# Optimization experiments

Measured on AMD Instinct MI355X. Metric: run time of the kernel, lower is better.

Reference implementation:

```python
import jax, jax.numpy as jnp
import numpy as np

B, H, W, DIM = 16, 64, 64, 512
GH, GW = 8, 8
NH = 16
HD = DIM // NH
POS = DIM // 16  # DynamicPosBias pos_dim = (dim//4)//4 = 32
EPS = 1e-5


def setup_inputs() -> dict:
    key = jax.random.key(0)
    ks = jax.random.split(key, 12)
    w = lambda k, s: jax.random.normal(k, s, jnp.float32) * 0.02
    f32 = jnp.float32
    return {
        "x": jax.random.normal(ks[0], (B, H * W, DIM), f32),
        "norm1_g": jnp.ones((DIM,), f32), "norm1_b": jnp.zeros((DIM,), f32),
        "qkv_w": w(ks[1], (3 * DIM, DIM)), "qkv_b": jnp.zeros((3 * DIM,), f32),
        "proj_w": w(ks[2], (DIM, DIM)), "proj_b": jnp.zeros((DIM,), f32),
        "pos_w0": w(ks[3], (POS, 2)), "pos_b0": jnp.zeros((POS,), f32),
        "pos_ln0_g": jnp.ones((POS,), f32), "pos_ln0_b": jnp.zeros((POS,), f32),
        "pos_w1": w(ks[4], (POS, POS)), "pos_b1": jnp.zeros((POS,), f32),
        "pos_ln1_g": jnp.ones((POS,), f32), "pos_ln1_b": jnp.zeros((POS,), f32),
        "pos_w2": w(ks[5], (POS, POS)), "pos_b2": jnp.zeros((POS,), f32),
        "pos_ln2_g": jnp.ones((POS,), f32), "pos_ln2_b": jnp.zeros((POS,), f32),
        "pos_w3": w(ks[6], (NH, POS)), "pos_b3": jnp.zeros((NH,), f32),
        "norm2_g": jnp.ones((DIM,), f32), "norm2_b": jnp.zeros((DIM,), f32),
        "mlp_w1": w(ks[7], (4 * DIM, DIM)), "mlp_b1": jnp.zeros((4 * DIM,), f32),
        "mlp_w2": w(ks[8], (DIM, 4 * DIM)), "mlp_b2": jnp.zeros((DIM,), f32),
    }


def _ln(x, g, b):
    m = jnp.mean(x, -1, keepdims=True)
    v = jnp.mean(jnp.square(x - m), -1, keepdims=True)
    return (x - m) * jax.lax.rsqrt(v + EPS) * g + b


def _rel_bias_tables():
    # relative coordinate table [(2GH-1)*(2GW-1), 2]
    ph = jnp.arange(1 - GH, GH)
    pw = jnp.arange(1 - GW, GW)
    biases = jnp.stack(jnp.meshgrid(ph, pw, indexing="ij")).reshape(2, -1).T.astype(jnp.float32)
    # relative position index [GH*GW, GH*GW]
    coords = jnp.stack(jnp.meshgrid(jnp.arange(GH), jnp.arange(GW), indexing="ij")).reshape(2, -1)
    rel = (coords[:, :, None] - coords[:, None, :]).transpose(1, 2, 0)  # [N,N,2]
    idx = (rel[..., 0] + GH - 1) * (2 * GW - 1) + (rel[..., 1] + GW - 1)
    return biases, idx


def reference(x, norm1_g, norm1_b, qkv_w, qkv_b, proj_w, proj_b,
              pos_w0, pos_b0, pos_ln0_g, pos_ln0_b,
              pos_w1, pos_b1, pos_ln1_g, pos_ln1_b,
              pos_w2, pos_b2, pos_ln2_g, pos_ln2_b,
              pos_w3, pos_b3, norm2_g, norm2_b,
              mlp_w1, mlp_b1, mlp_w2, mlp_b2):
    biases, rel_idx = _rel_bias_tables()
    Ng = GH * GW
    scale = HD ** -0.5

    shortcut = x
    h = _ln(x, norm1_g, norm1_b).reshape(B, H, W, DIM)
    # use_lda=True: long-distance (strided) grouping
    h = h.reshape(B, GH, H // GH, GW, W // GW, DIM).transpose(0, 2, 4, 1, 3, 5)
    h = h.reshape(B * (H * W) // Ng, Ng, DIM)  # [G, Ng, C]

    # attention
    qkv = h @ qkv_w.T + qkv_b
    qkv = qkv.reshape(-1, Ng, 3, NH, HD).transpose(2, 0, 3, 1, 4)  # [3,G,NH,Ng,HD]
    q, k, v = qkv[0], qkv[1], qkv[2]
    attn = jnp.einsum("ghnd,ghmd->ghnm", q * scale, k)

    # dynamic position bias MLP on the coordinate table
    p = jax.nn.relu(_ln(biases @ pos_w0.T + pos_b0, pos_ln0_g, pos_ln0_b))
    p = jax.nn.relu(_ln(p @ pos_w1.T + pos_b1, pos_ln1_g, pos_ln1_b))
    p = jax.nn.relu(_ln(p @ pos_w2.T + pos_b2, pos_ln2_g, pos_ln2_b))
    p = p @ pos_w3.T + pos_b3  # [(2GH-1)(2GW-1), NH]
    rel_bias = p[rel_idx].transpose(2, 0, 1)  # [NH, Ng, Ng]

    attn = jax.nn.softmax(attn + rel_bias[None], axis=-1)
    o = jnp.einsum("ghnm,ghmd->ghnd", attn, v)
    o = o.transpose(0, 2, 1, 3).reshape(-1, Ng, DIM)
    o = o @ proj_w.T + proj_b

    # ungroup (inverse of lda grouping)
    o = o.reshape(B, H // GH, W // GW, GH, GW, DIM)
    o = o.transpose(0, 3, 1, 4, 2, 5).reshape(B, H * W, DIM)

    x = shortcut + o
    m = _ln(x, norm2_g, norm2_b)
    m = jax.nn.gelu(m @ mlp_w1.T + mlp_b1, approximate=False)
    m = m @ mlp_w2.T + mlp_b2
    return x + m
```

## Files before the change

### kernel.cpp

```cpp
#include <hip/hip_runtime.h>
#include <hip/hip_bf16.h>

typedef __bf16 bf16;
typedef __bf16 bf16x8 __attribute__((ext_vector_type(8)));
typedef __bf16 bf16x4 __attribute__((ext_vector_type(4)));
typedef float f32x4_t __attribute__((ext_vector_type(4)));

static constexpr int kDIM = 512;

static constexpr size_t OFF_QKVW = 0;
static constexpr size_t OFF_PROJW = 1572864;
static constexpr size_t OFF_W1   = 2097152;
static constexpr size_t OFF_W2   = 4194304;
static constexpr size_t OFF_PTAB = 6291456;
static constexpr size_t OFF_A    = 8388608;
static constexpr size_t OFF_B    = 276824064;

typedef __attribute__((address_space(3))) uint32_t lds_u32_t;
typedef __attribute__((address_space(1))) const uint32_t glb_u32_t;
#define ASYNC_COPY16(gp, lp) __builtin_amdgcn_global_load_lds((glb_u32_t*)(gp), (lds_u32_t*)(lp), 16, 0, 0)
#define WAITV0() asm volatile("s_waitcnt vmcnt(0)" ::: "memory")

__global__ void cast_fp8_k(const float* __restrict__ in, unsigned char* __restrict__ out, int n4)
{
    int i = blockIdx.x * blockDim.x + threadIdx.x;
    if (i < n4) {
        float4 v = ((const float4*)in)[i];
        int p = __builtin_amdgcn_cvt_pk_fp8_f32(v.x * 64.0f, v.y * 64.0f, 0, false);
        p = __builtin_amdgcn_cvt_pk_fp8_f32(v.z * 64.0f, v.w * 64.0f, p, true);
        ((unsigned int*)out)[i] = (unsigned int)p;
    }
}

template<int GROUP>
__global__ __launch_bounds__(256)
void ln_k(const float* __restrict__ x, const float* __restrict__ gw,
          const float* __restrict__ bw, unsigned char* __restrict__ out)
{
    const int t = blockIdx.x * 4 + (threadIdx.x >> 6);
    const int lane = threadIdx.x & 63;
    const float* xp = x + (size_t)t * kDIM + lane * 8;
    float4 p0 = *(const float4*)xp;
    float4 p1 = *(const float4*)(xp + 4);
    float v[8] = {p0.x, p0.y, p0.z, p0.w, p1.x, p1.y, p1.z, p1.w};
    float s = 0.f;
#pragma unroll
    for (int i = 0; i < 8; ++i) s += v[i];
#pragma unroll
    for (int off = 32; off > 0; off >>= 1) s += __shfl_xor(s, off);
    const float mean = s * (1.0f / 512.0f);
    float q = 0.f;
#pragma unroll
    for (int i = 0; i < 8; ++i) { float d = v[i] - mean; q += d * d; }
#pragma unroll
    for (int off = 32; off > 0; off >>= 1) q += __shfl_xor(q, off);
    const float rstd = rsqrtf(q * (1.0f / 512.0f) + 1e-5f);
    size_t orow;
    if (GROUP) {
        int b = t >> 12, r = (t >> 6) & 63, c = t & 63;
        int g = b * 64 + (r & 7) * 8 + (c & 7);
        int n = (r >> 3) * 8 + (c >> 3);
        orow = (size_t)g * 64 + n;
    } else {
        orow = t;
    }
    float4 g0 = *(const float4*)(gw + lane * 8);
    float4 g1 = *(const float4*)(gw + lane * 8 + 4);
    float4 b0 = *(const float4*)(bw + lane * 8);
    float4 b1 = *(const float4*)(bw + lane * 8 + 4);
    float gg[8] = {g0.x, g0.y, g0.z, g0.w, g1.x, g1.y, g1.z, g1.w};
    float bb[8] = {b0.x, b0.y, b0.z, b0.w, b1.x, b1.y, b1.z, b1.w};
    float o[8];
#pragma unroll
    for (int i = 0; i < 8; ++i) o[i] = ((v[i] - mean) * rstd * gg[i] + bb[i]) * 32.0f;
    unsigned int lo = 0, hi = 0;
    lo = (unsigned int)__builtin_amdgcn_cvt_pk_fp8_f32(o[0], o[1], 0, false);
    lo = (unsigned int)__builtin_amdgcn_cvt_pk_fp8_f32(o[2], o[3], (int)lo, true);
    hi = (unsigned int)__builtin_amdgcn_cvt_pk_fp8_f32(o[4], o[5], 0, false);
    hi = (unsigned int)__builtin_amdgcn_cvt_pk_fp8_f32(o[6], o[7], (int)hi, true);
    uint2 u; u.x = lo; u.y = hi;
    *(uint2*)(out + orow * kDIM + lane * 8) = u;
}

__device__ inline void ln32_relu(float* h, const float* g, const float* b)
{
    float m = 0.f;
#pragma unroll
    for (int i = 0; i < 32; ++i) m += h[i];
    m *= (1.0f / 32.0f);
    float v = 0.f;
#pragma unroll
    for (int i = 0; i < 32; ++i) { float d = h[i] - m; v += d * d; }
    v *= (1.0f / 32.0f);
    float r = rsqrtf(v + 1e-5f);
#pragma unroll
    for (int i = 0; i < 32; ++i) h[i] = fmaxf((h[i] - m) * r * g[i] + b[i], 0.f);
}

__global__ __launch_bounds__(256)
void posmlp_k(const float* __restrict__ w0, const float* __restrict__ b0,
              const float* __restrict__ g0, const float* __restrict__ bb0,
              const float* __restrict__ w1, const float* __restrict__ b1,
              const float* __restrict__ g1, const float* __restrict__ bb1,
              const float* __restrict__ w2, const float* __restrict__ b2,
              const float* __restrict__ g2, const float* __restrict__ bb2,
              const float* __restrict__ w3, const float* __restrict__ b3,
              float* __restrict__ ptab)
{
    int r = threadIdx.x;
    if (r >= 225) return;
    float in0 = (float)(r / 15) - 7.0f;
    float in1 = (float)(r % 15) - 7.0f;
    float h[32], h2[32];
#pragma unroll
    for (int o = 0; o < 32; ++o) h[o] = w0[o * 2] * in0 + w0[o * 2 + 1] * in1 + b0[o];
    ln32_relu(h, g0, bb0);
#pragma unroll
    for (int o = 0; o < 32; ++o) {
        float s = b1[o];
#pragma unroll
        for (int i = 0; i < 32; ++i) s += w1[o * 32 + i] * h[i];
        h2[o] = s;
    }
    ln32_relu(h2, g1, bb1);
#pragma unroll
    for (int o = 0; o < 32; ++o) {
        float s = b2[o];
#pragma unroll
        for (int i = 0; i < 32; ++i) s += w2[o * 32 + i] * h2[i];
        h[o] = s;
    }
    ln32_relu(h, g2, bb2);
#pragma unroll
    for (int o = 0; o < 16; ++o) {
        float s = b3[o];
#pragma unroll
        for (int i = 0; i < 32; ++i) s += w3[o * 32 + i] * h[i];
        ptab[r * 16 + o] = s;
    }
}

__global__ __launch_bounds__(256)
void attn_mfma_k(const unsigned char* __restrict__ qkv, const float* __restrict__ ptab,
                 unsigned char* __restrict__ obuf)
{
    const int g  = blockIdx.x >> 1;
    const int hb = blockIdx.x & 1;
    const int w  = threadIdx.x >> 6;
    const int lane = threadIdx.x & 63;
    const int c = lane & 15, q = lane >> 4;

    __shared__ float ptl[16][240];
    __shared__ alignas(16) bf16 pl[4][4096];
    __shared__ alignas(16) bf16 vt[4][2048];

    for (int i = threadIdx.x; i < 3600; i += 256)
        ptl[i & 15][i >> 4] = ptab[i];
    __syncthreads();

    const size_t rowb = (size_t)g * 64;
    bf16* pw = pl[w];
    char* vw = (char*)vt[w];

    for (int hh = 0; hh < 2; ++hh) {
        const int head = hb * 8 + hh * 4 + w;
        const unsigned char* qb = qkv + rowb * 2048 + head * 32;

        const bf16* vbase = (const bf16*)(qb + 1024 + head * 32);
        bf16x8 vrow[4];
#pragma unroll
        for (int l = 0; l < 4; ++l)
            vrow[l] = *(const bf16x8*)((const bf16*)((const char*)vbase + (size_t)lane * 2048) + l * 8);

        long aq[4], bk[4];
#pragma unroll
        for (int i = 0; i < 4; ++i) {
            aq[i] = *(const long*)(qb + (size_t)(i * 16 + c) * 2048 + q * 8);
            bk[i] = *(const long*)(qb + 512 + (size_t)(i * 16 + c) * 2048 + q * 8);
        }

        f32x4_t s[4][4];
#pragma unroll
        for (int i = 0; i < 4; ++i)
#pragma unroll
            for (int j = 0; j < 4; ++j)
                s[i][j] = __builtin_amdgcn_mfma_f32_16x16x32_fp8_fp8(aq[i], bk[j],
                          (f32x4_t){0.f, 0.f, 0.f, 0.f}, 0, 0, 0);

#pragma unroll
        for (int l = 0; l < 4; ++l)
#pragma unroll
            for (int j = 0; j < 8; ++j) {
                const int d = l * 8 + j;
                *(bf16*)(vw + d * 128 + ((lane * 2) ^ ((d & 7) << 4))) = vrow[l][j];
            }

        const float scale = 0.17677669529663687f / 1024.0f;
        float inv[4][4];
#pragma unroll
        for (int i = 0; i < 4; ++i)
#pragma unroll
            for (int jj = 0; jj < 4; ++jj) {
                const int n = i * 16 + q * 4 + jj;
                const int na = n >> 3, nu = n & 7;
                float mx = -1e30f;
#pragma unroll
                for (int j = 0; j < 4; ++j) {
                    const int m = j * 16 + c;
                    const int idx = (na - (m >> 3) + 7) * 15 + (nu - (m & 7) + 7);
                    float v = s[i][j][jj] * scale + ptl[head][idx];
                    s[i][j][jj] = v;
                    mx = fmaxf(mx, v);
                }
#pragma unroll
                for (int off = 1; off < 16; off <<= 1) mx = fmaxf(mx, __shfl_xor(mx, off));
                float sum = 0.f;
#pragma unroll
                for (int j = 0; j < 4; ++j) {
                    float e = __expf(s[i][j][jj] - mx);
                    s[i][j][jj] = e; sum += e;
                }
#pragma unroll
                for (int off = 1; off < 16; off <<= 1) sum += __shfl_xor(sum, off);
                inv[i][jj] = 1.0f / sum;
            }

#pragma unroll
        for (int i = 0; i < 4; ++i)
#pragma unroll
            for (int jj = 0; jj < 4; ++jj) {
                const int n = i * 16 + q * 4 + jj;
                const int swz = (n & 7) << 4;
#pragma unroll
                for (int j = 0; j < 4; ++j) {
                    const int m = j * 16 + c;
                    *(bf16*)((char*)pw + n * 128 + ((m * 2) ^ swz)) = (bf16)s[i][j][jj];
                }
            }

        bf16x8 bv[2][2];
#pragma unroll
        for (int ks = 0; ks < 2; ++ks)
#pragma unroll
            for (int dt = 0; dt < 2; ++dt)
                bv[ks][dt] = *(const bf16x8*)(vw + (dt * 16 + c) * 128 +
                              ((ks * 64 + q * 16) ^ ((c & 7) << 4)));

        f32x4_t o[4][2];
#pragma unroll
        for (int i = 0; i < 4; ++i)
#pragma unroll
            for (int dt = 0; dt < 2; ++dt)
                o[i][dt] = (f32x4_t){0.f, 0.f, 0.f, 0.f};
#pragma unroll
        for (int ks = 0; ks < 2; ++ks)
#pragma unroll
            for (int i = 0; i < 4; ++i) {
                const int n = i * 16 + c;
                bf16x8 ap = *(const bf16x8*)((char*)pw + n * 128 +
                             ((ks * 64 + q * 16) ^ ((n & 7) << 4)));
#pragma unroll
                for (int dt = 0; dt < 2; ++dt)
                    o[i][dt] = __builtin_amdgcn_mfma_f32_16x16x32_bf16(ap, bv[ks][dt], o[i][dt], 0, 0, 0);
            }

        unsigned char* ob = obuf + rowb * 512 + head * 32;
#pragma unroll
        for (int i = 0; i < 4; ++i)
#pragma unroll
            for (int dt = 0; dt < 2; ++dt)
#pragma unroll
                for (int jj = 0; jj < 4; ++jj) {
                    const int n = i * 16 + q * 4 + jj;
                    float val = o[i][dt][jj] * inv[i][jj] * 32.0f;
                    int p8 = __builtin_amdgcn_cvt_pk_fp8_f32(val, val, 0, false);
                    ob[(size_t)n * 512 + dt * 16 + c] = (unsigned char)(p8 & 0xff);
                }
    }
}

template<int MODE, int NBX, int K>
__global__ __launch_bounds__(256, 2)
void gemm_fp8(const unsigned char* __restrict__ A, const unsigned char* __restrict__ Bw,
              const float* __restrict__ bias, const float* __restrict__ resid,
              void* __restrict__ outp, int N, float invs)
{
    __shared__ alignas(16) unsigned char As[128 * 128];
    __shared__ alignas(16) unsigned char Bs[128 * 128];
    const int tid = threadIdx.x;
    const int lane = tid & 63;
    const int w = tid >> 6;
    const int wr = w >> 1, wc = w & 1;
    const int c = lane & 15, q = lane >> 4;

    const int bid = blockIdx.y * NBX + blockIdx.x;
    const int nwg = gridDim.y * NBX;
    const int swz = (bid & 7) * (nwg >> 3) + (bid >> 3);
    const int by = swz / NBX;
    const int bx = swz - by * NBX;
    const int rowBase = by * 128;
    const int colBase = bx * 128;

    f32x4_t acc[4][4];
#pragma unroll
    for (int m = 0; m < 4; ++m)
#pragma unroll
        for (int n = 0; n < 4; ++n)
            acc[m][n] = (f32x4_t){0.f, 0.f, 0.f, 0.f};

    const int key = c & 7;
    const int hb8 = (q & 1) * 8;

    const unsigned char* aSrc[4];
    const unsigned char* bSrc[4];
    int ldsOff[4];
#pragma unroll
    for (int l = 0; l < 4; ++l) {
        const int cg = l * 256 + tid;
        const int row = cg >> 3;
        const int sg = (cg & 7) ^ (row & 7);
        aSrc[l] = A + (size_t)(rowBase + row) * K + sg * 16;
        bSrc[l] = Bw + (size_t)(colBase + row) * K + sg * 16;
        ldsOff[l] = (l * 256 + (tid & 192)) * 16;
    }
    int sbo[4];
#pragma unroll
    for (int kk = 0; kk < 4; ++kk)
        sbo[kk] = (((2 * kk + (q >> 1)) ^ key) << 4) + hb8;

#pragma unroll
    for (int kt = 0; kt < K; kt += 128) {
#pragma unroll
        for (int l = 0; l < 4; ++l) {
            ASYNC_COPY16(aSrc[l] + kt, As + ldsOff[l]);
            ASYNC_COPY16(bSrc[l] + kt, Bs + ldsOff[l]);
        }
        WAITV0();
        __syncthreads();
#pragma unroll
        for (int kk = 0; kk < 4; ++kk) {
            const int sb = sbo[kk];
            long af[4], bfr[4];
#pragma unroll
            for (int m = 0; m < 4; ++m) {
                const int row = wr * 64 + m * 16 + c;
                af[m] = *(const long*)((const char*)As + row * 128 + sb);
            }
#pragma unroll
            for (int n = 0; n < 4; ++n) {
                const int row = wc * 64 + n * 16 + c;
                bfr[n] = *(const long*)((const char*)Bs + row * 128 + sb);
            }
#pragma unroll
            for (int m = 0; m < 4; ++m)
#pragma unroll
                for (int n = 0; n < 4; ++n)
                    acc[m][n] = __builtin_amdgcn_mfma_f32_16x16x32_fp8_fp8(af[m], bfr[n], acc[m][n], 0, 0, 0);
        }
        __syncthreads();
    }

#pragma unroll
    for (int m = 0; m < 4; ++m) {
#pragma unroll
        for (int jj = 0; jj < 4; ++jj) {
            int grow = rowBase + wr * 64 + m * 16 + q * 4 + jj;
#pragma unroll
            for (int n = 0; n < 4; ++n) {
                int gcol = colBase + wc * 64 + n * 16 + c;
                float v = acc[m][n][jj] * invs + bias[gcol];
                if constexpr (MODE == 0) {
                    char* ob = (char*)outp;
                    if (gcol < 1024) {
                        int p8 = __builtin_amdgcn_cvt_pk_fp8_f32(v * 32.0f, v * 32.0f, 0, false);
                        ob[(size_t)grow * 2048 + gcol] = (char)(p8 & 0xff);
                    } else {
                        *(bf16*)(ob + (size_t)grow * 2048 + 1024 + (size_t)(gcol - 1024) * 2) = (bf16)v;
                    }
                } else if constexpr (MODE == 1) {
                    float e = __expf(1.5957691216057308f * (v + 0.044715f * v * v * v));
                    v = v * (e / (1.0f + e));
                    int p8 = __builtin_amdgcn_cvt_pk_fp8_f32(v * 64.0f, v * 64.0f, 0, false);
                    ((unsigned char*)outp)[(size_t)grow * N + gcol] = (unsigned char)(p8 & 0xff);
                } else if constexpr (MODE == 2) {
                    int g = grow >> 6, ns = grow & 63;
                    int b = g >> 6, i = (g >> 3) & 7, j = g & 7;
                    int a = ns >> 3, u = ns & 7;
                    int t = b * 4096 + (a * 8 + i) * 64 + (u * 8 + j);
                    size_t oi = (size_t)t * 512 + gcol;
                    ((float*)outp)[oi] = resid[oi] + v;
                } else {
                    size_t oi = (size_t)grow * 512 + gcol;
                    ((float*)outp)[oi] = resid[oi] + v;
                }
            }
        }
    }
}

extern "C" void kernel_launch(void* const* d_in, const int* in_sizes, int n_in,
                              void* d_out, int out_size, void* d_ws, size_t ws_size,
                              hipStream_t stream)
{
    const float* x    = (const float*)d_in[0];
    const float* n1g  = (const float*)d_in[1];
    const float* n1b  = (const float*)d_in[2];
    const float* qkvw = (const float*)d_in[3];
    const float* qkvb = (const float*)d_in[4];
    const float* pjw  = (const float*)d_in[5];
    const float* pjb  = (const float*)d_in[6];
    const float* pw0  = (const float*)d_in[7];
    const float* pb0  = (const float*)d_in[8];
    const float* pg0  = (const float*)d_in[9];
    const float* pbb0 = (const float*)d_in[10];
    const float* pw1  = (const float*)d_in[11];
    const float* pb1  = (const float*)d_in[12];
    const float* pg1  = (const float*)d_in[13];
    const float* pbb1 = (const float*)d_in[14];
    const float* pw2  = (const float*)d_in[15];
    const float* pb2  = (const float*)d_in[16];
    const float* pg2  = (const float*)d_in[17];
    const float* pbb2 = (const float*)d_in[18];
    const float* pw3  = (const float*)d_in[19];
    const float* pb3  = (const float*)d_in[20];
    const float* n2g  = (const float*)d_in[21];
    const float* n2b  = (const float*)d_in[22];
    const float* w1   = (const float*)d_in[23];
    const float* b1   = (const float*)d_in[24];
    const float* w2   = (const float*)d_in[25];
    const float* b2   = (const float*)d_in[26];

    char* ws = (char*)d_ws;
    unsigned char* qkvw_f8 = (unsigned char*)(ws + OFF_QKVW);
    unsigned char* pjw_f8  = (unsigned char*)(ws + OFF_PROJW);
    unsigned char* w1_f8 = (unsigned char*)(ws + OFF_W1);
    unsigned char* w2_f8 = (unsigned char*)(ws + OFF_W2);
    float* ptab  = (float*)(ws + OFF_PTAB);
    unsigned char* bufA8 = (unsigned char*)(ws + OFF_A);
    unsigned char* bufB8 = (unsigned char*)(ws + OFF_B);
    float* xout  = (float*)d_out;

    cast_fp8_k<<<(1536 * 512 / 4 + 255) / 256, 256, 0, stream>>>(qkvw, qkvw_f8, 1536 * 512 / 4);
    cast_fp8_k<<<(512 * 512 / 4 + 255) / 256, 256, 0, stream>>>(pjw, pjw_f8, 512 * 512 / 4);
    cast_fp8_k<<<(2048 * 512 / 4 + 255) / 256, 256, 0, stream>>>(w1, w1_f8, 2048 * 512 / 4);
    cast_fp8_k<<<(512 * 2048 / 4 + 255) / 256, 256, 0, stream>>>(w2, w2_f8, 512 * 2048 / 4);

    posmlp_k<<<1, 256, 0, stream>>>(pw0, pb0, pg0, pbb0, pw1, pb1, pg1, pbb1,
                                    pw2, pb2, pg2, pbb2, pw3, pb3, ptab);

    ln_k<1><<<16384, 256, 0, stream>>>(x, n1g, n1b, bufB8);

    gemm_fp8<0, 12, 512><<<dim3(12, 512), 256, 0, stream>>>(bufB8, qkvw_f8, qkvb, nullptr,
                                                            bufA8, 1536, 1.0f / 2048.0f);

    attn_mfma_k<<<2048, 256, 0, stream>>>(bufA8, ptab, bufB8);

    gemm_fp8<2, 4, 512><<<dim3(4, 512), 256, 0, stream>>>(bufB8, pjw_f8, pjb, x,
                                                          xout, 512, 1.0f / 2048.0f);

    ln_k<0><<<16384, 256, 0, stream>>>(xout, n2g, n2b, bufB8);

    gemm_fp8<1, 16, 512><<<dim3(16, 512), 256, 0, stream>>>(bufB8, w1_f8, b1, nullptr,
                                                            bufA8, 2048, 1.0f / 2048.0f);

    gemm_fp8<3, 4, 2048><<<dim3(4, 512), 256, 0, stream>>>(bufA8, w2_f8, b2, xout,
                                                           xout, 512, 1.0f / 4096.0f);
}
```

Before: 688.3 us.

## Pack FC1 GELU output as 4-byte fp8 stores via permuted hidden layout

The FC1 GEMM epilogue now packs four fp8 GELU outputs per thread into one 32-bit store instead of four single-byte stores. This permutes the hidden-dimension column order within 64-column blocks. To keep the result correct, the w2 weight is cast to fp8 with the matching column permutation, so FC2 reduces over the same permuted K order. The GEMM's async-copy address setup is also simplified to a single base pointer plus strides, which saves a few registers. The cost is a slower scattered byte-store weight cast kernel for w2.

```diff
diff --git a/kernel.cpp b/kernel.cpp
--- a/kernel.cpp
+++ b/kernel.cpp
@@ -29,6 +29,26 @@
         int p = __builtin_amdgcn_cvt_pk_fp8_f32(v.x * 64.0f, v.y * 64.0f, 0, false);
         p = __builtin_amdgcn_cvt_pk_fp8_f32(v.z * 64.0f, v.w * 64.0f, p, true);
         ((unsigned int*)out)[i] = (unsigned int)p;
+    }
+}
+
+__global__ void cast_fp8_perm_k(const float* __restrict__ in, unsigned char* __restrict__ out,
+                                int n4, int ncols)
+{
+    int i = blockIdx.x * blockDim.x + threadIdx.x;
+    if (i < n4) {
+        float4 v = ((const float4*)in)[i];
+        int idx = i * 4;
+        int row = idx / ncols;
+        int j0 = idx - row * ncols;
+        float vv[4] = {v.x, v.y, v.z, v.w};
+#pragma unroll
+        for (int t = 0; t < 4; ++t) {
+            int j = j0 + t;
+            int pj = (j & ~127) | (j & 64) | ((j & 15) << 2) | ((j >> 4) & 3);
+            int p8 = __builtin_amdgcn_cvt_pk_fp8_f32(vv[t] * 64.0f, vv[t] * 64.0f, 0, false);
+            out[(size_t)row * ncols + pj] = (unsigned char)(p8 & 0xff);
+        }
     }
 }
 
@@ -311,18 +331,12 @@
     const int key = c & 7;
     const int hb8 = (q & 1) * 8;
 
-    const unsigned char* aSrc[4];
-    const unsigned char* bSrc[4];
-    int ldsOff[4];
-#pragma unroll
-    for (int l = 0; l < 4; ++l) {
-        const int cg = l * 256 + tid;
-        const int row = cg >> 3;
-        const int sg = (cg & 7) ^ (row & 7);
-        aSrc[l] = A + (size_t)(rowBase + row) * K + sg * 16;
-        bSrc[l] = Bw + (size_t)(colBase + row) * K + sg * 16;
-        ldsOff[l] = (l * 256 + (tid & 192)) * 16;
-    }
+    const int sg = (tid & 7) ^ ((tid >> 3) & 7);
+    const unsigned char* aBase = A + (size_t)(rowBase + (tid >> 3)) * K + sg * 16;
+    const unsigned char* bBase = Bw + (size_t)(colBase + (tid >> 3)) * K + sg * 16;
+    unsigned char* ldsA = As + (tid & 192) * 16;
+    unsigned char* ldsB = Bs + (tid & 192) * 16;
+
     int sbo[4];
 #pragma unroll
     for (int kk = 0; kk < 4; ++kk)
@@ -332,8 +346,8 @@
     for (int kt = 0; kt < K; kt += 128) {
 #pragma unroll
         for (int l = 0; l < 4; ++l) {
-            ASYNC_COPY16(aSrc[l] + kt, As + ldsOff[l]);
-            ASYNC_COPY16(bSrc[l] + kt, Bs + ldsOff[l]);
+            ASYNC_COPY16(aBase + (size_t)l * 32 * K + kt, ldsA + l * 4096);
+            ASYNC_COPY16(bBase + (size_t)l * 32 * K + kt, ldsB + l * 4096);
         }
         WAITV0();
         __syncthreads();
@@ -365,33 +379,45 @@
 #pragma unroll
         for (int jj = 0; jj < 4; ++jj) {
             int grow = rowBase + wr * 64 + m * 16 + q * 4 + jj;
-#pragma unroll
-            for (int n = 0; n < 4; ++n) {
-                int gcol = colBase + wc * 64 + n * 16 + c;
-                float v = acc[m][n][jj] * invs + bias[gcol];
-                if constexpr (MODE == 0) {
-                    char* ob = (char*)outp;
-                    if (gcol < 1024) {
-                        int p8 = __builtin_amdgcn_cvt_pk_fp8_f32(v * 32.0f, v * 32.0f, 0, false);
-                        ob[(size_t)grow * 2048 + gcol] = (char)(p8 & 0xff);
+            float vv[4];
+#pragma unroll
+            for (int n = 0; n < 4; ++n)
+                vv[n] = acc[m][n][jj] * invs + bias[colBase + wc * 64 + n * 16 + c];
+            if constexpr (MODE == 1) {
+#pragma unroll
+                for (int n = 0; n < 4; ++n) {
+                    float v = vv[n];
+                    float e = __expf(1.5957691216057308f * (v + 0.044715f * v * v * v));
+                    vv[n] = v * (e / (1.0f + e)) * 64.0f;
+                }
+                int p = __builtin_amdgcn_cvt_pk_fp8_f32(vv[0], vv[1], 0, false);
+                p = __builtin_amdgcn_cvt_pk_fp8_f32(vv[2], vv[3], p, true);
+                *(unsigned int*)((char*)outp + (size_t)grow * N + colBase + wc * 64 + c * 4) =
+                    (unsigned int)p;
+            } else {
+#pragma unroll
+                for (int n = 0; n < 4; ++n) {
+                    int gcol = colBase + wc * 64 + n * 16 + c;
+                    float v = vv[n];
+                    if constexpr (MODE == 0) {
+                        char* ob = (char*)outp;
+                        if (gcol < 1024) {
+                            int p8 = __builtin_amdgcn_cvt_pk_fp8_f32(v * 32.0f, v * 32.0f, 0, false);
+                            ob[(size_t)grow * 2048 + gcol] = (char)(p8 & 0xff);
+                        } else {
+                            *(bf16*)(ob + (size_t)grow * 2048 + 1024 + (size_t)(gcol - 1024) * 2) = (bf16)v;
+                        }
+                    } else if constexpr (MODE == 2) {
+                        int g = grow >> 6, ns = grow & 63;
+                        int b = g >> 6, i = (g >> 3) & 7, j = g & 7;
+                        int a = ns >> 3, u = ns & 7;
+                        int t = b * 4096 + (a * 8 + i) * 64 + (u * 8 + j);
+                        size_t oi = (size_t)t * 512 + gcol;
+                        ((float*)outp)[oi] = resid[oi] + v;
                     } else {
-                        *(bf16*)(ob + (size_t)grow * 2048 + 1024 + (size_t)(gcol - 1024) * 2) = (bf16)v;
+                        size_t oi = (size_t)grow * 512 + gcol;
+                        ((float*)outp)[oi] = resid[oi] + v;
                     }
-                } else if constexpr (MODE == 1) {
-                    float e = __expf(1.5957691216057308f * (v + 0.044715f * v * v * v));
-                    v = v * (e / (1.0f + e));
-                    int p8 = __builtin_amdgcn_cvt_pk_fp8_f32(v * 64.0f, v * 64.0f, 0, false);
-                    ((unsigned char*)outp)[(size_t)grow * N + gcol] = (unsigned char)(p8 & 0xff);
-                } else if constexpr (MODE == 2) {
-                    int g = grow >> 6, ns = grow & 63;
-                    int b = g >> 6, i = (g >> 3) & 7, j = g & 7;
-                    int a = ns >> 3, u = ns & 7;
-                    int t = b * 4096 + (a * 8 + i) * 64 + (u * 8 + j);
-                    size_t oi = (size_t)t * 512 + gcol;
-                    ((float*)outp)[oi] = resid[oi] + v;
-                } else {
-                    size_t oi = (size_t)grow * 512 + gcol;
-                    ((float*)outp)[oi] = resid[oi] + v;
                 }
             }
         }
@@ -443,7 +469,7 @@
     cast_fp8_k<<<(1536 * 512 / 4 + 255) / 256, 256, 0, stream>>>(qkvw, qkvw_f8, 1536 * 512 / 4);
     cast_fp8_k<<<(512 * 512 / 4 + 255) / 256, 256, 0, stream>>>(pjw, pjw_f8, 512 * 512 / 4);
     cast_fp8_k<<<(2048 * 512 / 4 + 255) / 256, 256, 0, stream>>>(w1, w1_f8, 2048 * 512 / 4);
-    cast_fp8_k<<<(512 * 2048 / 4 + 255) / 256, 256, 0, stream>>>(w2, w2_f8, 512 * 2048 / 4);
+    cast_fp8_perm_k<<<(512 * 2048 / 4 + 255) / 256, 256, 0, stream>>>(w2, w2_f8, 512 * 2048 / 4, 2048);
 
     posmlp_k<<<1, 256, 0, stream>>>(pw0, pb0, pg0, pbb0, pw1, pb1, pg1, pbb1,
                                     pw2, pb2, pg2, pbb2, pw3, pb3, ptab);
```

Result: no change. 691.1 us (+0.4%).
